# Kernel optimization log

Hardware: AMD Instinct MI355X
Metric: run time of the kernel (lower is better)

Reference implementation:

```python
import jax, jax.numpy as jnp
import numpy as np

B, S, D = 4, 4096, 64

def setup_inputs() -> dict:
    key = jax.random.key(0)
    kq, kk, kv = jax.random.split(key, 3)
    q = jax.random.normal(kq, (B, S, D), dtype=jnp.float32)
    k = jax.random.normal(kk, (B, S, D), dtype=jnp.float32)
    v = jax.random.normal(kv, (B, S, D), dtype=jnp.float32)
    return {"q": q, "k": k, "v": v}

def reference(q, k, v):
    # unnormalized attention: scores [b,i,j], then weighted sum over j
    attn = jnp.einsum('bid,bjd->bij', q, k)
    out = jnp.einsum('bij,bjd->bid', attn, v)
    return out
```

## Files before the change

### kernel.cpp

```cpp
#include <hip/hip_runtime.h>
#include <hip/hip_bf16.h>


#define BATCH 4
#define SEQ   4096
#define DIM   64
#define CH    128
#define NB    (BATCH * SEQ / CH)
#define PERB  (NB / BATCH)

typedef float f4  __attribute__((ext_vector_type(4)));
typedef short bf16x8 __attribute__((ext_vector_type(8)));
typedef float f32x4  __attribute__((ext_vector_type(4)));

__device__ inline unsigned short f2bf(float f) {
    union { float f; unsigned u; } v; v.f = f;
    unsigned r = (v.u + 0x7fffu + ((v.u >> 16) & 1u)) >> 16;
    return (unsigned short)r;
}

__global__ __launch_bounds__(256) void k1_ktv(const float* __restrict__ K,
                                              const float* __restrict__ V,
                                              float* __restrict__ part,
                                              unsigned short* __restrict__ MB,
                                              unsigned int* __restrict__ cnt) {
    __shared__ f4 Ks[2048];
    __shared__ f4 Vs[2048];
    __shared__ int lastFlag;
    const int bx = blockIdx.x;
    const int t  = threadIdx.x;
    const int b  = bx / PERB;

    const f4* Kg = (const f4*)(K + (size_t)bx * (CH * DIM));
    const f4* Vg = (const f4*)(V + (size_t)bx * (CH * DIM));
#pragma unroll
    for (int i = 0; i < 8; ++i) {
        Ks[t + 256 * i] = Kg[t + 256 * i];
        Vs[t + 256 * i] = Vg[t + 256 * i];
    }
    __syncthreads();

    const int rg = t >> 4;
    const int cg = t & 15;
    f4 a0 = 0.f, a1 = 0.f, a2 = 0.f, a3 = 0.f;
#pragma unroll 8
    for (int j = 0; j < CH; ++j) {
        f4 a = Ks[j * 16 + rg];
        f4 v = Vs[j * 16 + cg];
        a0 += v * a.x;
        a1 += v * a.y;
        a2 += v * a.z;
        a3 += v * a.w;
    }
    f4* P = (f4*)part + (size_t)bx * 1024;
    P[(rg * 4 + 0) * 16 + cg] = a0;
    P[(rg * 4 + 1) * 16 + cg] = a1;
    P[(rg * 4 + 2) * 16 + cg] = a2;
    P[(rg * 4 + 3) * 16 + cg] = a3;

    __syncthreads();
    if (t == 0) {
        __threadfence();
        unsigned old = atomicAdd(&cnt[b], 1u);
        unsigned u = old + 1u;
        lastFlag = (u == (unsigned)PERB) || (u == 0xAAAAAAAAu + (unsigned)PERB);
    }
    __syncthreads();

    if (lastFlag) {
        __threadfence();
        const f4* Pb = (const f4*)part + (size_t)b * PERB * 1024;
#pragma unroll
        for (int i = 0; i < 4; ++i) {
            const int s = t + 256 * i;
            f4 acc = 0.f;
#pragma unroll 8
            for (int p = 0; p < PERB; ++p)
                acc += Pb[p * 1024 + s];
            const int dp = s >> 4;
            const int ks = dp >> 5, quad = (dp >> 3) & 3, jj = dp & 7;
            const int cbase = (s & 15) * 4;
#pragma unroll
            for (int q = 0; q < 4; ++q) {
                const int c = cbase + q, ct = c >> 4, m = c & 15;
                MB[(((b * 8 + ct * 2 + ks) * 64) + quad * 16 + m) * 8 + jj] = f2bf(acc[q]);
            }
        }
    }
}

__global__ __launch_bounds__(256) void k3_qm(const float* __restrict__ Q,
                                             const unsigned short* __restrict__ MB,
                                             float* __restrict__ out) {
    const int bx = blockIdx.x;
    const int t  = threadIdx.x;
    const int wave = t >> 6, lane = t & 63;
    const int m = lane & 15, quad = lane >> 4;
    const int b = bx >> 6;
    const int row0 = (bx & 63) * 64 + wave * 16;

    const float* qrow = Q + ((size_t)b * SEQ + row0 + m) * DIM;
    bf16x8 afrag[2];
#pragma unroll
    for (int ks = 0; ks < 2; ++ks) {
        const f4* qp = (const f4*)(qrow + ks * 32 + quad * 8);
        f4 q1 = qp[0], q2 = qp[1];
        bf16x8 a;
        a[0] = (short)f2bf(q1.x); a[1] = (short)f2bf(q1.y);
        a[2] = (short)f2bf(q1.z); a[3] = (short)f2bf(q1.w);
        a[4] = (short)f2bf(q2.x); a[5] = (short)f2bf(q2.y);
        a[6] = (short)f2bf(q2.z); a[7] = (short)f2bf(q2.w);
        afrag[ks] = a;
    }

    const bf16x8* MBv = (const bf16x8*)MB + (size_t)b * 8 * 64;
    f32x4 acc[4];
#pragma unroll
    for (int ct = 0; ct < 4; ++ct) acc[ct] = (f32x4)0.f;
#pragma unroll
    for (int ct = 0; ct < 4; ++ct)
#pragma unroll
        for (int ks = 0; ks < 2; ++ks) {
            bf16x8 bfrag = MBv[(ct * 2 + ks) * 64 + lane];
            acc[ct] = __builtin_amdgcn_mfma_f32_16x16x32_bf16(afrag[ks], bfrag, acc[ct], 0, 0, 0);
        }

    float* orow = out + ((size_t)b * SEQ + row0) * DIM;
#pragma unroll
    for (int ct = 0; ct < 4; ++ct)
#pragma unroll
        for (int r = 0; r < 4; ++r)
            orow[(quad * 4 + r) * DIM + ct * 16 + m] = acc[ct][r];
}

extern "C" void kernel_launch(void* const* d_in, const int* in_sizes, int n_in,
                              void* d_out, int out_size, void* d_ws, size_t ws_size,
                              hipStream_t stream) {
    const float* q = (const float*)d_in[0];
    const float* k = (const float*)d_in[1];
    const float* v = (const float*)d_in[2];
    float* out = (float*)d_out;

    float* part = (float*)d_ws;
    unsigned short* MB = (unsigned short*)((char*)d_ws + (size_t)2 * 1024 * 1024);
    unsigned int* cnt = (unsigned int*)((char*)d_ws + (size_t)2 * 1024 * 1024 + 32 * 1024);

    k1_ktv<<<NB, 256, 0, stream>>>(k, v, part, MB, cnt);
    k3_qm<<<BATCH * 64, 256, 0, stream>>>(q, MB, out);
}
```

Measured before the change: 86.04 us.

## Move partial reduction into Q kernel and drop last-block atomic reduction

The K^T·V kernel now covers 256 rows per block in four staged 64-row chunks, which halves the block count and the number of partials. The atomic counter and last-block reduction are removed. Each block of the second kernel now reduces the 16 per-batch partials itself, converts the result to bf16 in the MFMA layout in shared memory, and then does the Q·M product. This takes the serial last-block reduction off the critical path and frees the first kernel from its counter. The cost is that each of the 256 Q blocks redundantly reads 16 partials of 16 KB each.

New measurement: 80.29 us. 1.07x faster.

```diff
diff --git a/kernel.cpp b/kernel.cpp
--- a/kernel.cpp
+++ b/kernel.cpp
@@ -5,9 +5,9 @@
 #define BATCH 4
 #define SEQ   4096
 #define DIM   64
-#define CH    128
-#define NB    (BATCH * SEQ / CH)
-#define PERB  (NB / BATCH)
+#define CH    256
+#define NB1   (BATCH * SEQ / CH)
+#define PERB  (NB1 / BATCH)
 
 typedef float f4  __attribute__((ext_vector_type(4)));
 typedef short bf16x8 __attribute__((ext_vector_type(8)));
@@ -21,82 +21,71 @@
 
 __global__ __launch_bounds__(256) void k1_ktv(const float* __restrict__ K,
                                               const float* __restrict__ V,
-                                              float* __restrict__ part,
-                                              unsigned short* __restrict__ MB,
-                                              unsigned int* __restrict__ cnt) {
-    __shared__ f4 Ks[2048];
-    __shared__ f4 Vs[2048];
-    __shared__ int lastFlag;
+                                              float* __restrict__ part) {
+    __shared__ f4 Ks[1024];
+    __shared__ f4 Vs[1024];
     const int bx = blockIdx.x;
     const int t  = threadIdx.x;
-    const int b  = bx / PERB;
-
-    const f4* Kg = (const f4*)(K + (size_t)bx * (CH * DIM));
-    const f4* Vg = (const f4*)(V + (size_t)bx * (CH * DIM));
-#pragma unroll
-    for (int i = 0; i < 8; ++i) {
-        Ks[t + 256 * i] = Kg[t + 256 * i];
-        Vs[t + 256 * i] = Vg[t + 256 * i];
-    }
-    __syncthreads();
-
     const int rg = t >> 4;
     const int cg = t & 15;
     f4 a0 = 0.f, a1 = 0.f, a2 = 0.f, a3 = 0.f;
+#pragma unroll
+    for (int sc = 0; sc < 4; ++sc) {
+        const f4* Kg = (const f4*)(K + ((size_t)bx * CH + sc * 64) * DIM);
+        const f4* Vg = (const f4*)(V + ((size_t)bx * CH + sc * 64) * DIM);
+        if (sc) __syncthreads();
+#pragma unroll
+        for (int i = 0; i < 4; ++i) {
+            Ks[t + 256 * i] = Kg[t + 256 * i];
+            Vs[t + 256 * i] = Vg[t + 256 * i];
+        }
+        __syncthreads();
 #pragma unroll 8
-    for (int j = 0; j < CH; ++j) {
-        f4 a = Ks[j * 16 + rg];
-        f4 v = Vs[j * 16 + cg];
-        a0 += v * a.x;
-        a1 += v * a.y;
-        a2 += v * a.z;
-        a3 += v * a.w;
+        for (int j = 0; j < 64; ++j) {
+            f4 a = Ks[j * 16 + rg];
+            f4 v = Vs[j * 16 + cg];
+            a0 += v * a.x;
+            a1 += v * a.y;
+            a2 += v * a.z;
+            a3 += v * a.w;
+        }
     }
     f4* P = (f4*)part + (size_t)bx * 1024;
     P[(rg * 4 + 0) * 16 + cg] = a0;
     P[(rg * 4 + 1) * 16 + cg] = a1;
     P[(rg * 4 + 2) * 16 + cg] = a2;
     P[(rg * 4 + 3) * 16 + cg] = a3;
+}
 
-    __syncthreads();
-    if (t == 0) {
-        __threadfence();
-        unsigned old = atomicAdd(&cnt[b], 1u);
-        unsigned u = old + 1u;
-        lastFlag = (u == (unsigned)PERB) || (u == 0xAAAAAAAAu + (unsigned)PERB);
+__global__ __launch_bounds__(256) void k2_qm(const float* __restrict__ Q,
+                                             const float* __restrict__ part,
+                                             float* __restrict__ out) {
+    __shared__ unsigned short MBs[4096];
+    const int bx = blockIdx.x;
+    const int t  = threadIdx.x;
+    const int b  = bx >> 6;
+
+    const f4* Pb = (const f4*)part + (size_t)b * PERB * 1024;
+#pragma unroll
+    for (int i = 0; i < 4; ++i) {
+        const int s = t + 256 * i;
+        f4 acc = 0.f;
+#pragma unroll
+        for (int p = 0; p < PERB; ++p)
+            acc += Pb[p * 1024 + s];
+        const int k  = s >> 4;
+        const int ks = k >> 5, quad = (k >> 3) & 3, j = k & 7;
+        const int cbase = (s & 15) * 4;
+#pragma unroll
+        for (int q = 0; q < 4; ++q) {
+            const int c = cbase + q, ct = c >> 4, m = c & 15;
+            MBs[(((ct * 2 + ks) * 64) + quad * 16 + m) * 8 + j] = f2bf(acc[q]);
+        }
     }
     __syncthreads();
 
-    if (lastFlag) {
-        __threadfence();
-        const f4* Pb = (const f4*)part + (size_t)b * PERB * 1024;
-#pragma unroll
-        for (int i = 0; i < 4; ++i) {
-            const int s = t + 256 * i;
-            f4 acc = 0.f;
-#pragma unroll 8
-            for (int p = 0; p < PERB; ++p)
-                acc += Pb[p * 1024 + s];
-            const int dp = s >> 4;
-            const int ks = dp >> 5, quad = (dp >> 3) & 3, jj = dp & 7;
-            const int cbase = (s & 15) * 4;
-#pragma unroll
-            for (int q = 0; q < 4; ++q) {
-                const int c = cbase + q, ct = c >> 4, m = c & 15;
-                MB[(((b * 8 + ct * 2 + ks) * 64) + quad * 16 + m) * 8 + jj] = f2bf(acc[q]);
-            }
-        }
-    }
-}
-
-__global__ __launch_bounds__(256) void k3_qm(const float* __restrict__ Q,
-                                             const unsigned short* __restrict__ MB,
-                                             float* __restrict__ out) {
-    const int bx = blockIdx.x;
-    const int t  = threadIdx.x;
     const int wave = t >> 6, lane = t & 63;
     const int m = lane & 15, quad = lane >> 4;
-    const int b = bx >> 6;
     const int row0 = (bx & 63) * 64 + wave * 16;
 
     const float* qrow = Q + ((size_t)b * SEQ + row0 + m) * DIM;
@@ -113,7 +102,7 @@
         afrag[ks] = a;
     }
 
-    const bf16x8* MBv = (const bf16x8*)MB + (size_t)b * 8 * 64;
+    const bf16x8* MBv = (const bf16x8*)MBs;
     f32x4 acc[4];
 #pragma unroll
     for (int ct = 0; ct < 4; ++ct) acc[ct] = (f32x4)0.f;
@@ -140,11 +129,8 @@
     const float* k = (const float*)d_in[1];
     const float* v = (const float*)d_in[2];
     float* out = (float*)d_out;
+    float* part = (float*)d_ws;
 
-    float* part = (float*)d_ws;
-    unsigned short* MB = (unsigned short*)((char*)d_ws + (size_t)2 * 1024 * 1024);
-    unsigned int* cnt = (unsigned int*)((char*)d_ws + (size_t)2 * 1024 * 1024 + 32 * 1024);
-
-    k1_ktv<<<NB, 256, 0, stream>>>(k, v, part, MB, cnt);
-    k3_qm<<<BATCH * 64, 256, 0, stream>>>(q, MB, out);
+    k1_ktv<<<NB1, 256, 0, stream>>>(k, v, part);
+    k2_qm<<<BATCH * 64, 256, 0, stream>>>(q, part, out);
 }
```
